# Kernel optimization log

Hardware: AMD Instinct MI355X
Metric: run time of the kernel (lower is better)

Reference implementation:

```python
import jax, jax.numpy as jnp
import numpy as np

VOCAB, EMB, HID = 50000, 256, 512
H = HID // 2            # per-direction hidden size
K = 24                  # tagset size
START, STOP = 22, 23
B, T = 32, 512
NEG = -10000.0


def setup_inputs():
    key = jax.random.key(0)
    ks = jax.random.split(key, 16)
    s = 0.1  # weight scale to keep gates in a sane range
    sentence = jax.random.randint(ks[0], (B, T), 0, VOCAB)
    embedding = jax.random.normal(ks[1], (VOCAB, EMB), jnp.float32)
    w_ih_f = jax.random.normal(ks[2], (4 * H, EMB), jnp.float32) * s
    w_hh_f = jax.random.normal(ks[3], (4 * H, H), jnp.float32) * s
    b_ih_f = jax.random.normal(ks[4], (4 * H,), jnp.float32) * s
    b_hh_f = jax.random.normal(ks[5], (4 * H,), jnp.float32) * s
    w_ih_b = jax.random.normal(ks[6], (4 * H, EMB), jnp.float32) * s
    w_hh_b = jax.random.normal(ks[7], (4 * H, H), jnp.float32) * s
    b_ih_b = jax.random.normal(ks[8], (4 * H,), jnp.float32) * s
    b_hh_b = jax.random.normal(ks[9], (4 * H,), jnp.float32) * s
    w_out = jax.random.normal(ks[10], (K, HID), jnp.float32) * s
    b_out = jax.random.normal(ks[11], (K,), jnp.float32) * s
    transitions = jax.random.normal(ks[12], (K, K), jnp.float32)
    transitions = transitions.at[START, :].set(NEG).at[:, STOP].set(NEG)
    h0 = jax.random.normal(ks[13], (2, B, H), jnp.float32)  # [fwd,bwd] initial h
    c0 = jax.random.normal(ks[14], (2, B, H), jnp.float32)  # [fwd,bwd] initial c
    return {"sentence": sentence, "embedding": embedding,
            "w_ih_f": w_ih_f, "w_hh_f": w_hh_f, "b_ih_f": b_ih_f, "b_hh_f": b_hh_f,
            "w_ih_b": w_ih_b, "w_hh_b": w_hh_b, "b_ih_b": b_ih_b, "b_hh_b": b_hh_b,
            "w_out": w_out, "b_out": b_out, "transitions": transitions,
            "h0": h0, "c0": c0}


def _lstm_dir(x_tbe, w_ih, w_hh, b_ih, b_hh, h0, c0, reverse):
    # x_tbe: [T, B, E]; PyTorch gate order i, f, g, o
    def step(carry, x_t):
        h, c = carry
        gates = x_t @ w_ih.T + b_ih + h @ w_hh.T + b_hh  # [B, 4H]
        i, f, g, o = jnp.split(gates, 4, axis=-1)
        c = jax.nn.sigmoid(f) * c + jax.nn.sigmoid(i) * jnp.tanh(g)
        h = jax.nn.sigmoid(o) * jnp.tanh(c)
        return (h, c), h
    _, hs = jax.lax.scan(step, (h0, c0), x_tbe, reverse=reverse)
    return hs  # [T, B, H]


def _viterbi(feats_tbk, transitions):
    # feats_tbk: [T, B, K]; transitions[next, prev]
    init = jnp.full((B, K), NEG, feats_tbk.dtype).at[:, START].set(0.0)

    def step(fv, feat_t):
        scores = fv[:, None, :] + transitions[None, :, :]  # [B, next, prev]
        bp = jnp.argmax(scores, axis=-1)                   # [B, K]
        fv_new = jnp.max(scores, axis=-1) + feat_t
        return fv_new, bp

    fv, bps = jax.lax.scan(step, init, feats_tbk)  # bps: [T, B, K]
    terminal = fv + transitions[STOP][None, :]
    last_tag = jnp.argmax(terminal, axis=-1)       # [B]
    path_score = jnp.max(terminal, axis=-1)        # [B]

    def back(tag, bp_t):
        prev = jnp.take_along_axis(bp_t, tag[:, None], axis=1)[:, 0]
        return prev, tag
    # process t = T-1 .. 0; carry holds tag at time t, emits it, steps to t-1
    _, path = jax.lax.scan(back, last_tag, bps, reverse=True)  # [T, B]
    return path_score, path.T.astype(jnp.int32)  # [B], [B, T]


def reference(sentence, embedding, w_ih_f, w_hh_f, b_ih_f, b_hh_f,
              w_ih_b, w_hh_b, b_ih_b, b_hh_b, w_out, b_out,
              transitions, h0, c0):
    emb = embedding[sentence]                       # [B, T, EMB]
    x = jnp.transpose(emb, (1, 0, 2))               # [T, B, EMB]
    hf = _lstm_dir(x, w_ih_f, w_hh_f, b_ih_f, b_hh_f, h0[0], c0[0], False)
    hb = _lstm_dir(x, w_ih_b, w_hh_b, b_ih_b, b_hh_b, h0[1], c0[1], True)
    hs = jnp.concatenate([hf, hb], axis=-1)         # [T, B, HID]
    feats = hs @ w_out.T + b_out                    # [T, B, K]
    score, path = _viterbi(feats, transitions)
    return score, path
```

## Files before the change

### kernel.cpp

```cpp
#include <hip/hip_runtime.h>

#define T_LEN 512
#define BATCH 32
#define HDIR  256
#define KTAG  24
#define START_TAG 22
#define STOP_TAG  23
#define NEGV  (-10000.0f)
#define SENTU 0x7FC0DEADu

typedef float vf4 __attribute__((ext_vector_type(4)));

#define XPROJ_OFF   0ull
#define XPROJ_ELEMS (2ull*512*1024*32)
#define FEATS_OFF   (XPROJ_OFF + XPROJ_ELEMS)
#define FEATS_ELEMS (512ull*32*24)
#define HIST_OFF    (FEATS_OFF + FEATS_ELEMS)
#define HIST_ELEMS  (2ull*513*8192)

#define BARRIER_LGKM() asm volatile("s_waitcnt lgkmcnt(0)\n\ts_barrier" ::: "memory")

__device__ __forceinline__ float fsig(float x) {
  return __builtin_amdgcn_rcpf(1.0f + __expf(-x));
}
__device__ __forceinline__ float ftanh(float x) {
  return 2.0f * __builtin_amdgcn_rcpf(1.0f + __expf(-2.0f * x)) - 1.0f;
}
__device__ __forceinline__ unsigned um(unsigned a, unsigned b) { return a < b ? a : b; }

__global__ void k_fill(float* __restrict__ p, int n4) {
  int i = blockIdx.x * blockDim.x + threadIdx.x;
  if (i < n4) {
    float* dst = p + (size_t)i * 4;
    const float sv = __uint_as_float(SENTU);
    vf4 v; v.x = sv; v.y = sv; v.z = sv; v.w = sv;
    asm volatile("global_store_dwordx4 %0, %1, off sc0 sc1"
                 :: "v"(dst), "v"(v) : "memory");
  }
}

__global__ __launch_bounds__(256, 1) void k_main(
    const int* __restrict__ sent, const float* __restrict__ emb,
    const float* __restrict__ wihf, const float* __restrict__ wihb,
    const float* __restrict__ bihf, const float* __restrict__ bhhf,
    const float* __restrict__ bihb, const float* __restrict__ bhhb,
    const float* __restrict__ whhf, const float* __restrict__ whhb,
    const float* __restrict__ h0, const float* __restrict__ c0,
    float* __restrict__ xproj, float* __restrict__ hist)
{
  extern __shared__ float dynpad[];
  __shared__ float As[16][132];
  __shared__ float Bs[16][132];
  __shared__ int   sid[128];
  __shared__ float hl[32 * 256];
  const int bid = blockIdx.x;
  const int tid = threadIdx.x;
  if (sent == (const int*)0) dynpad[0] = 0.f;

  if (bid >= 64) {
    const int idx = bid - 64;
    const int mt_rank = idx >> 4;
    const int sub = idx & 15;
    const int y = sub >> 1;
    const int dir = sub & 1;
    const int mt = (mt_rank & 1) ? (127 - (mt_rank >> 1)) : (mt_rank >> 1);
    const int m0 = mt * 128;
    const int n0 = y * 128;
    const float* __restrict__ W = dir ? wihb : wihf;
    if (tid < 128) {
      int m = m0 + tid;
      sid[tid] = sent[(m & 31) * 512 + (m >> 5)];
    }
    __syncthreads();
    float acc[8][8];
#pragma unroll
    for (int i = 0; i < 8; ++i)
#pragma unroll
      for (int j = 0; j < 8; ++j) acc[i][j] = 0.f;
    const int r = tid >> 1, qq = tid & 1;
    const int ty = tid >> 4, tx = tid & 15;
    for (int k0 = 0; k0 < 256; k0 += 16) {
      const float* ap = &emb[(size_t)sid[r] * 256 + k0 + qq * 8];
      const float* bp = &W[(size_t)(n0 + r) * 256 + k0 + qq * 8];
      float4 a0 = *(const float4*)ap;
      float4 a1 = *(const float4*)(ap + 4);
      float4 b0 = *(const float4*)bp;
      float4 b1 = *(const float4*)(bp + 4);
      __syncthreads();
      As[qq*8+0][r] = a0.x; As[qq*8+1][r] = a0.y; As[qq*8+2][r] = a0.z; As[qq*8+3][r] = a0.w;
      As[qq*8+4][r] = a1.x; As[qq*8+5][r] = a1.y; As[qq*8+6][r] = a1.z; As[qq*8+7][r] = a1.w;
      Bs[qq*8+0][r] = b0.x; Bs[qq*8+1][r] = b0.y; Bs[qq*8+2][r] = b0.z; Bs[qq*8+3][r] = b0.w;
      Bs[qq*8+4][r] = b1.x; Bs[qq*8+5][r] = b1.y; Bs[qq*8+6][r] = b1.z; Bs[qq*8+7][r] = b1.w;
      __syncthreads();
#pragma unroll
      for (int kk = 0; kk < 16; ++kk) {
        float4 av0 = *(const float4*)&As[kk][ty*8];
        float4 av1 = *(const float4*)&As[kk][ty*8+4];
        float4 bv0 = *(const float4*)&Bs[kk][tx*8];
        float4 bv1 = *(const float4*)&Bs[kk][tx*8+4];
        float am[8] = {av0.x,av0.y,av0.z,av0.w,av1.x,av1.y,av1.z,av1.w};
        float bn[8] = {bv0.x,bv0.y,bv0.z,bv0.w,bv1.x,bv1.y,bv1.z,bv1.w};
#pragma unroll
        for (int i = 0; i < 8; ++i)
#pragma unroll
          for (int j = 0; j < 8; ++j)
            acc[i][j] = fmaf(am[i], bn[j], acc[i][j]);
      }
    }
    const float* bi_p = dir ? bihb : bihf;
    const float* bh_p = dir ? bhhb : bhhf;
    float bias[8];
#pragma unroll
    for (int j = 0; j < 8; ++j) { int n = n0 + tx*8 + j; bias[j] = bi_p[n] + bh_p[n]; }
    const int mb = m0 + ty * 8;
    const int tt = mb >> 5, bb = mb & 31;
#pragma unroll
    for (int j = 0; j < 8; ++j) {
      int n = n0 + tx*8 + j;
      float* dst = &xproj[((((size_t)dir*512 + tt)*1024) + n)*32 + bb];
      vf4 o0, o1;
      o0[0] = acc[0][j]+bias[j]; o0[1] = acc[1][j]+bias[j];
      o0[2] = acc[2][j]+bias[j]; o0[3] = acc[3][j]+bias[j];
      o1[0] = acc[4][j]+bias[j]; o1[1] = acc[5][j]+bias[j];
      o1[2] = acc[6][j]+bias[j]; o1[3] = acc[7][j]+bias[j];
      asm volatile(
        "global_store_dwordx4 %0, %2, off sc0 sc1\n\t"
        "global_store_dwordx4 %1, %3, off sc0 sc1"
        :: "v"(dst), "v"(dst + 4), "v"(o0), "v"(o1) : "memory");
    }
    return;
  }

  const int dir = bid >> 5;
  const int slice = bid & 31;
  const int rowg = tid >> 5;
  const int bgrp = (tid >> 3) & 3;
  const int kgrp = tid & 7;
  const int jg = slice * 8 + rowg;
  const float* __restrict__ W = dir ? whhb : whhf;

  float2 w2[4][16];
#pragma unroll
  for (int g = 0; g < 4; ++g)
#pragma unroll
    for (int kk2 = 0; kk2 < 16; ++kk2)
      w2[g][kk2] = *(const float2*)&W[(size_t)(g*256 + jg)*256 + kgrp*32 + 2*kk2];

  float cc[8];
#pragma unroll
  for (int bi = 0; bi < 8; ++bi)
    cc[bi] = c0[(size_t)(dir*32 + bgrp*8 + bi)*256 + jg];

  const int kk = tid & 31;
  const int base_col = tid & ~31;
  const int kw4 = 4*((tid >> 5) & 7);
  const int rot = (4*kgrp + 2*bgrp) & 31;
  float* const histd = hist + (size_t)dir * 513 * 8192;
  float hnew[8];

  for (int s = 0; s < 512; ++s) {
    const int t = dir ? (511 - s) : s;

    vf4 hv[8];
    if (s == 0) {
#pragma unroll
      for (int q = 0; q < 8; ++q)
#pragma unroll
        for (int bl = 0; bl < 4; ++bl)
          hv[q][bl] = h0[(size_t)(dir*32 + 4*q + bl)*256 + tid];
    } else {
      const float* sp = histd + (size_t)s*8192 + (size_t)tid*4;
      const float* p0 = sp;
      const float* p1 = sp + 1024;
      const float* p2 = sp + 2048;
      const float* p3 = sp + 3072;
      const float* p4 = sp + 4096;
      const float* p5 = sp + 5120;
      const float* p6 = sp + 6144;
      const float* p7 = sp + 7168;
      while (true) {
        asm volatile(
          "global_load_dwordx4 %0, %1, off sc0 sc1\n\t"
          "s_waitcnt vmcnt(0)"
          : "=&v"(hv[7]) : "v"(p7) : "memory");
        unsigned z = 0xFFFFFFFFu;
#pragma unroll
        for (int bl = 0; bl < 4; ++bl)
          z = um(z, __float_as_uint(hv[7][bl]) ^ SENTU);
        if (z) break;
        __builtin_amdgcn_s_sleep(1);
      }
      while (true) {
        asm volatile(
          "global_load_dwordx4 %0, %7, off sc0 sc1\n\t"
          "global_load_dwordx4 %1, %8, off sc0 sc1\n\t"
          "global_load_dwordx4 %2, %9, off sc0 sc1\n\t"
          "global_load_dwordx4 %3, %10, off sc0 sc1\n\t"
          "global_load_dwordx4 %4, %11, off sc0 sc1\n\t"
          "global_load_dwordx4 %5, %12, off sc0 sc1\n\t"
          "global_load_dwordx4 %6, %13, off sc0 sc1\n\t"
          "s_waitcnt vmcnt(0)"
          : "=&v"(hv[0]), "=&v"(hv[1]), "=&v"(hv[2]), "=&v"(hv[3]),
            "=&v"(hv[4]), "=&v"(hv[5]), "=&v"(hv[6])
          : "v"(p0), "v"(p1), "v"(p2), "v"(p3),
            "v"(p4), "v"(p5), "v"(p6)
          : "memory");
        unsigned z = 0xFFFFFFFFu;
#pragma unroll
        for (int q = 0; q < 7; ++q)
#pragma unroll
          for (int bl = 0; bl < 4; ++bl)
            z = um(z, __float_as_uint(hv[q][bl]) ^ SENTU);
        if (z) break;
        __builtin_amdgcn_s_sleep(1);
      }
    }

    vf4 xv0, xv1, xv2, xv3, xv4, xv5, xv6, xv7;
    const float* xb = &xproj[((((size_t)dir*512 + t)*1024) + jg)*32 + bgrp*8];
    const float* xa0 = xb;             const float* xa1 = xb + 4;
    const float* xa2 = xb + 8192;      const float* xa3 = xb + 8196;
    const float* xa4 = xb + 16384;     const float* xa5 = xb + 16388;
    const float* xa6 = xb + 24576;     const float* xa7 = xb + 24580;
    if (kgrp == 0) {
      asm volatile(
        "global_load_dwordx4 %0, %8, off sc0 sc1\n\t"
        "global_load_dwordx4 %1, %9, off sc0 sc1\n\t"
        "global_load_dwordx4 %2, %10, off sc0 sc1\n\t"
        "global_load_dwordx4 %3, %11, off sc0 sc1\n\t"
        "global_load_dwordx4 %4, %12, off sc0 sc1\n\t"
        "global_load_dwordx4 %5, %13, off sc0 sc1\n\t"
        "global_load_dwordx4 %6, %14, off sc0 sc1\n\t"
        "global_load_dwordx4 %7, %15, off sc0 sc1"
        : "=&v"(xv0), "=&v"(xv1), "=&v"(xv2), "=&v"(xv3),
          "=&v"(xv4), "=&v"(xv5), "=&v"(xv6), "=&v"(xv7)
        : "v"(xa0), "v"(xa1), "v"(xa2), "v"(xa3),
          "v"(xa4), "v"(xa5), "v"(xa6), "v"(xa7)
        : "memory");
    }

#pragma unroll
    for (int q = 0; q < 8; ++q) {
      const int rwq = (kw4 + 2*((q >> 1) & 3)) & 31;
      const int col = base_col + ((kk + rwq) & 31);
#pragma unroll
      for (int bl = 0; bl < 4; ++bl)
        hl[(4*q + bl)*256 + col] = hv[q][bl];
    }
    BARRIER_LGKM();

    float acc[4][8];
#pragma unroll
    for (int g = 0; g < 4; ++g)
#pragma unroll
      for (int bi = 0; bi < 8; ++bi) acc[g][bi] = 0.f;

    const int hbase = kgrp * 32;
#pragma unroll
    for (int kk2 = 0; kk2 < 16; ++kk2) {
      const int idx = hbase + ((2*kk2 + rot) & 31);
      float2 h2[8];
#pragma unroll
      for (int bi = 0; bi < 8; ++bi)
        h2[bi] = *(const float2*)&hl[(bgrp*8 + bi)*256 + idx];
#pragma unroll
      for (int g = 0; g < 4; ++g)
#pragma unroll
        for (int bi = 0; bi < 8; ++bi) {
          acc[g][bi] = fmaf(w2[g][kk2].x, h2[bi].x, acc[g][bi]);
          acc[g][bi] = fmaf(w2[g][kk2].y, h2[bi].y, acc[g][bi]);
        }
    }

    if (kgrp == 0) {
      asm volatile("s_waitcnt vmcnt(0)"
                   : "+v"(xv0), "+v"(xv1), "+v"(xv2), "+v"(xv3),
                     "+v"(xv4), "+v"(xv5), "+v"(xv6), "+v"(xv7)
                   :: "memory");
      while (true) {
        unsigned z = 0xFFFFFFFFu;
#pragma unroll
        for (int bl = 0; bl < 4; ++bl) {
          z = um(z, __float_as_uint(xv0[bl]) ^ SENTU);
          z = um(z, __float_as_uint(xv1[bl]) ^ SENTU);
          z = um(z, __float_as_uint(xv2[bl]) ^ SENTU);
          z = um(z, __float_as_uint(xv3[bl]) ^ SENTU);
          z = um(z, __float_as_uint(xv4[bl]) ^ SENTU);
          z = um(z, __float_as_uint(xv5[bl]) ^ SENTU);
          z = um(z, __float_as_uint(xv6[bl]) ^ SENTU);
          z = um(z, __float_as_uint(xv7[bl]) ^ SENTU);
        }
        if (z) break;
        __builtin_amdgcn_s_sleep(1);
        asm volatile(
          "global_load_dwordx4 %0, %8, off sc0 sc1\n\t"
          "global_load_dwordx4 %1, %9, off sc0 sc1\n\t"
          "global_load_dwordx4 %2, %10, off sc0 sc1\n\t"
          "global_load_dwordx4 %3, %11, off sc0 sc1\n\t"
          "global_load_dwordx4 %4, %12, off sc0 sc1\n\t"
          "global_load_dwordx4 %5, %13, off sc0 sc1\n\t"
          "global_load_dwordx4 %6, %14, off sc0 sc1\n\t"
          "global_load_dwordx4 %7, %15, off sc0 sc1\n\t"
          "s_waitcnt vmcnt(0)"
          : "=&v"(xv0), "=&v"(xv1), "=&v"(xv2), "=&v"(xv3),
            "=&v"(xv4), "=&v"(xv5), "=&v"(xv6), "=&v"(xv7)
          : "v"(xa0), "v"(xa1), "v"(xa2), "v"(xa3),
            "v"(xa4), "v"(xa5), "v"(xa6), "v"(xa7)
          : "memory");
      }
      acc[0][0]+=xv0[0]; acc[0][1]+=xv0[1]; acc[0][2]+=xv0[2]; acc[0][3]+=xv0[3];
      acc[0][4]+=xv1[0]; acc[0][5]+=xv1[1]; acc[0][6]+=xv1[2]; acc[0][7]+=xv1[3];
      acc[1][0]+=xv2[0]; acc[1][1]+=xv2[1]; acc[1][2]+=xv2[2]; acc[1][3]+=xv2[3];
      acc[1][4]+=xv3[0]; acc[1][5]+=xv3[1]; acc[1][6]+=xv3[2]; acc[1][7]+=xv3[3];
      acc[2][0]+=xv4[0]; acc[2][1]+=xv4[1]; acc[2][2]+=xv4[2]; acc[2][3]+=xv4[3];
      acc[2][4]+=xv5[0]; acc[2][5]+=xv5[1]; acc[2][6]+=xv5[2]; acc[2][7]+=xv5[3];
      acc[3][0]+=xv6[0]; acc[3][1]+=xv6[1]; acc[3][2]+=xv6[2]; acc[3][3]+=xv6[3];
      acc[3][4]+=xv7[0]; acc[3][5]+=xv7[1]; acc[3][6]+=xv7[2]; acc[3][7]+=xv7[3];
    }
#pragma unroll
    for (int g = 0; g < 4; ++g)
#pragma unroll
      for (int bi = 0; bi < 8; ++bi) {
        float v = acc[g][bi];
        v += __shfl_xor(v, 1, 64);
        v += __shfl_xor(v, 2, 64);
        v += __shfl_xor(v, 4, 64);
        acc[g][bi] = v;
      }

#pragma unroll
    for (int bi = 0; bi < 8; ++bi) {
      float ig = fsig(acc[0][bi]);
      float fg = fsig(acc[1][bi]);
      float gg = ftanh(acc[2][bi]);
      float og = fsig(acc[3][bi]);
      cc[bi] = fg * cc[bi] + ig * gg;
      hnew[bi] = og * ftanh(cc[bi]);
    }

    if (kgrp == 0) {
      float* dp  = histd + (size_t)(s + 1)*8192 + ((size_t)(2*bgrp)*256 + jg)*4;
      float* dp2 = dp + 1024;
      vf4 s0; s0.x = hnew[0]; s0.y = hnew[1]; s0.z = hnew[2]; s0.w = hnew[3];
      vf4 s1; s1.x = hnew[4]; s1.y = hnew[5]; s1.z = hnew[6]; s1.w = hnew[7];
      asm volatile(
        "global_store_dwordx4 %0, %2, off sc0 sc1\n\t"
        "global_store_dwordx4 %1, %3, off sc0 sc1"
        :: "v"(dp), "v"(dp2), "v"(s0), "v"(s1) : "memory");
    }

    BARRIER_LGKM();
  }
}

__global__ __launch_bounds__(256) void k_feats(
    const float* __restrict__ hist, const float* __restrict__ wout,
    const float* __restrict__ bout, float* __restrict__ feats)
{
  const int t = blockIdx.x;
  const int tid = threadIdx.x;
  __shared__ float hlds[32 * 516];
#pragma unroll
  for (int dir = 0; dir < 2; ++dir) {
    const int slot = dir ? (512 - t) : (t + 1);
    const float* sp = hist + ((size_t)dir*513 + slot)*8192;
#pragma unroll
    for (int q = 0; q < 8; ++q) {
      vf4 v = *(const vf4*)&sp[(size_t)(q*256 + tid)*4];
      float* d = &hlds[(4*q)*516 + dir*256 + tid];
      d[0*516] = v.x; d[1*516] = v.y; d[2*516] = v.z; d[3*516] = v.w;
    }
  }
  __syncthreads();
  const int b = tid >> 3, ks = tid & 7;
#pragma unroll
  for (int kt = 0; kt < 3; ++kt) {
    int k = kt * 8 + ks;
    float acc = bout[k];
    const float* wr = wout + (size_t)k * 512;
#pragma unroll 8
    for (int kk = 0; kk < 512; kk += 4) {
      float4 h4 = *(const float4*)&hlds[b * 516 + kk];
      float4 w4 = *(const float4*)&wr[kk];
      acc += h4.x*w4.x + h4.y*w4.y + h4.z*w4.z + h4.w*w4.w;
    }
    feats[((size_t)t * 32 + b) * 24 + k] = acc;
  }
}

__global__ __launch_bounds__(64) void k_viterbi(
    const float* __restrict__ feats, const float* __restrict__ trans,
    float* __restrict__ out)
{
  const int b = blockIdx.x;
  const int lane = threadIdx.x;
  const int k = lane;
  __shared__ float fvl[2][32];
  __shared__ float pathb[512];
  __shared__ unsigned char bcol[512 * 24];
  float trr[24];
  if (k < 24) {
#pragma unroll
    for (int pv = 0; pv < 24; ++pv) trr[pv] = trans[k * 24 + pv];
  }
  if (k < 32) fvl[0][k] = (k == START_TAG) ? 0.f : NEGV;
  if (k < 32) fvl[1][k] = NEGV;
  __syncthreads();
  float fcur = (k < 24) ? feats[b * 24 + k] : 0.f;
  int q = 0;
  for (int t = 0; t < 512; ++t) {
    float fnext = (t < 511 && k < 24) ? feats[(size_t)(t + 1) * 768 + b * 24 + k] : 0.f;
    float fvp[24];
    {
      const float4* fp4 = (const float4*)&fvl[q][0];
#pragma unroll
      for (int i = 0; i < 6; ++i) {
        float4 v = fp4[i];
        fvp[i*4+0] = v.x; fvp[i*4+1] = v.y; fvp[i*4+2] = v.z; fvp[i*4+3] = v.w;
      }
    }
    float best = -3.4e38f; int bp = 0;
#pragma unroll
    for (int pv = 0; pv < 24; ++pv) {
      float v = fvp[pv] + trr[pv];
      if (v > best) { best = v; bp = pv; }
    }
    if (k < 24) {
      fvl[q ^ 1][k] = best + fcur;
      bcol[t * 24 + k] = (unsigned char)bp;
    }
    fcur = fnext;
    q ^= 1;
    __syncthreads();
  }
  if (lane == 0) {
    float best = -3.4e38f; int bt = 0;
#pragma unroll
    for (int kk = 0; kk < 24; ++kk) {
      float v = fvl[q][kk] + trans[STOP_TAG * 24 + kk];
      if (v > best) { best = v; bt = kk; }
    }
    out[b] = best;
    pathb[511] = (float)bt;
    int tag = bt;
    for (int t = 511; t >= 1; --t) {
      tag = bcol[t * 24 + tag];
      pathb[t - 1] = (float)tag;
    }
  }
  __syncthreads();
#pragma unroll
  for (int it = 0; it < 8; ++it)
    out[32 + (size_t)b * 512 + it * 64 + lane] = pathb[it * 64 + lane];
}

extern "C" void kernel_launch(void* const* d_in, const int* in_sizes, int n_in,
                              void* d_out, int out_size, void* d_ws, size_t ws_size,
                              hipStream_t stream) {
  (void)in_sizes; (void)n_in; (void)out_size; (void)ws_size;
  const int*   sent = (const int*)d_in[0];
  const float* emb  = (const float*)d_in[1];
  const float* wihf = (const float*)d_in[2];
  const float* whhf = (const float*)d_in[3];
  const float* bihf = (const float*)d_in[4];
  const float* bhhf = (const float*)d_in[5];
  const float* wihb = (const float*)d_in[6];
  const float* whhb = (const float*)d_in[7];
  const float* bihb = (const float*)d_in[8];
  const float* bhhb = (const float*)d_in[9];
  const float* wout = (const float*)d_in[10];
  const float* bout = (const float*)d_in[11];
  const float* trans= (const float*)d_in[12];
  const float* h0   = (const float*)d_in[13];
  const float* c0   = (const float*)d_in[14];

  float* ws     = (float*)d_ws;
  float* xproj  = ws + XPROJ_OFF;
  float* feats  = ws + FEATS_OFF;
  float* hist   = ws + HIST_OFF;

  const int n4 = (int)((XPROJ_ELEMS + FEATS_ELEMS + HIST_ELEMS) / 4);
  k_fill<<<(n4 + 255) / 256, 256, 0, stream>>>(ws, n4);
  k_main<<<2112, 256, 32768, stream>>>(sent, emb, wihf, wihb,
                                       bihf, bhhf, bihb, bhhb,
                                       whhf, whhb, h0, c0, xproj, hist);
  k_feats<<<512, 256, 0, stream>>>(hist, wout, bout, feats);
  k_viterbi<<<32, 64, 0, stream>>>(feats, trans, (float*)d_out);
}
```

Baseline: 4.387 ms.

## Fuse output projection into persistent kernel and replace sentinel-fill of xproj with per-tile flags

Moves the hidden-to-tag projection into extra blocks of the main persistent kernel. These blocks spin on the history buffer and compute feats as each timestep's forward and backward states become available, overlapping with the recurrence. The recurrent blocks no longer poll every xproj element for a sentinel. Instead, each GEMM tile writes a completion flag into the unused hist slot-0 region, and readers poll that flag every four timesteps. This lets the fill kernel touch only hist instead of the large xproj buffer. The change also register-prefetches the next K-slice in the input-projection GEMM, at the cost of more spin-polling blocks and extra resident work competing with the latency-critical recurrence.

```diff
diff --git a/kernel.cpp b/kernel.cpp
--- a/kernel.cpp
+++ b/kernel.cpp
@@ -46,18 +46,20 @@
     const float* __restrict__ bihb, const float* __restrict__ bhhb,
     const float* __restrict__ whhf, const float* __restrict__ whhb,
     const float* __restrict__ h0, const float* __restrict__ c0,
-    float* __restrict__ xproj, float* __restrict__ hist)
+    const float* __restrict__ wout, const float* __restrict__ bout,
+    float* __restrict__ xproj, float* __restrict__ feats,
+    float* __restrict__ hist)
 {
   extern __shared__ float dynpad[];
-  __shared__ float As[16][132];
-  __shared__ float Bs[16][132];
-  __shared__ int   sid[128];
-  __shared__ float hl[32 * 256];
+  __shared__ float smem[12544];
   const int bid = blockIdx.x;
   const int tid = threadIdx.x;
   if (sent == (const int*)0) dynpad[0] = 0.f;
 
-  if (bid >= 64) {
+  if (bid >= 64 && bid < 2112) {
+    float (*As)[132] = (float (*)[132])(smem);
+    float (*Bs)[132] = (float (*)[132])(smem + 2112);
+    int* sid = (int*)(smem + 4224);
     const int idx = bid - 64;
     const int mt_rank = idx >> 4;
     const int sub = idx & 15;
@@ -79,19 +81,27 @@
       for (int j = 0; j < 8; ++j) acc[i][j] = 0.f;
     const int r = tid >> 1, qq = tid & 1;
     const int ty = tid >> 4, tx = tid & 15;
+    const float* ap = &emb[(size_t)sid[r] * 256 + qq * 8];
+    const float* bp = &W[(size_t)(n0 + r) * 256 + qq * 8];
+    float4 a0 = *(const float4*)(ap);
+    float4 a1 = *(const float4*)(ap + 4);
+    float4 b0 = *(const float4*)(bp);
+    float4 b1 = *(const float4*)(bp + 4);
     for (int k0 = 0; k0 < 256; k0 += 16) {
-      const float* ap = &emb[(size_t)sid[r] * 256 + k0 + qq * 8];
-      const float* bp = &W[(size_t)(n0 + r) * 256 + k0 + qq * 8];
-      float4 a0 = *(const float4*)ap;
-      float4 a1 = *(const float4*)(ap + 4);
-      float4 b0 = *(const float4*)bp;
-      float4 b1 = *(const float4*)(bp + 4);
       __syncthreads();
       As[qq*8+0][r] = a0.x; As[qq*8+1][r] = a0.y; As[qq*8+2][r] = a0.z; As[qq*8+3][r] = a0.w;
       As[qq*8+4][r] = a1.x; As[qq*8+5][r] = a1.y; As[qq*8+6][r] = a1.z; As[qq*8+7][r] = a1.w;
       Bs[qq*8+0][r] = b0.x; Bs[qq*8+1][r] = b0.y; Bs[qq*8+2][r] = b0.z; Bs[qq*8+3][r] = b0.w;
       Bs[qq*8+4][r] = b1.x; Bs[qq*8+5][r] = b1.y; Bs[qq*8+6][r] = b1.z; Bs[qq*8+7][r] = b1.w;
       __syncthreads();
+      if (k0 + 16 < 256) {
+        const float* ap2 = ap + k0 + 16;
+        const float* bp2 = bp + k0 + 16;
+        a0 = *(const float4*)(ap2);
+        a1 = *(const float4*)(ap2 + 4);
+        b0 = *(const float4*)(bp2);
+        b1 = *(const float4*)(bp2 + 4);
+      }
 #pragma unroll
       for (int kk = 0; kk < 16; ++kk) {
         float4 av0 = *(const float4*)&As[kk][ty*8];
@@ -128,9 +138,94 @@
         "global_store_dwordx4 %1, %3, off sc0 sc1"
         :: "v"(dst), "v"(dst + 4), "v"(o0), "v"(o1) : "memory");
     }
+    asm volatile("s_waitcnt vmcnt(0)" ::: "memory");
+    __syncthreads();
+    if (tid == 0) {
+      float* fp = hist + (size_t)dir * 1024 + (size_t)mt * 8 + y;
+      const float z = 0.f;
+      asm volatile("global_store_dword %0, %1, off sc0 sc1"
+                   :: "v"(fp), "v"(z) : "memory");
+    }
     return;
   }
 
+  if (bid >= 2112) {
+    const int f = bid - 2112;
+    const int t = (f & 1) ? (256 + (f >> 1)) : (255 - (f >> 1));
+    float* hlds = smem;
+    const float* sF = hist + ((size_t)0*513 + (t + 1)) * 8192;
+    const float* sB = hist + ((size_t)1*513 + (512 - t)) * 8192;
+    {
+      const int p = tid & 31;
+      const float* pp = (((tid >> 5) & 1) ? sB : sF) + 32 * p;
+      while (true) {
+        float v;
+        asm volatile("global_load_dword %0, %1, off sc0 sc1\n\ts_waitcnt vmcnt(0)"
+                     : "=&v"(v) : "v"(pp) : "memory");
+        int bad = (__float_as_uint(v) == SENTU) ? 1 : 0;
+        if (!__any(bad)) break;
+        __builtin_amdgcn_s_sleep(64);
+      }
+    }
+    const int b = tid >> 3, ks = tid & 7;
+    float accv[3];
+    for (int dir2 = 0; dir2 < 2; ++dir2) {
+      const float* sp = (dir2 ? sB : sF) + (size_t)tid * 4;
+      vf4 v[8];
+      while (true) {
+        asm volatile(
+          "global_load_dwordx4 %0, %8, off sc0 sc1\n\t"
+          "global_load_dwordx4 %1, %9, off sc0 sc1\n\t"
+          "global_load_dwordx4 %2, %10, off sc0 sc1\n\t"
+          "global_load_dwordx4 %3, %11, off sc0 sc1\n\t"
+          "global_load_dwordx4 %4, %12, off sc0 sc1\n\t"
+          "global_load_dwordx4 %5, %13, off sc0 sc1\n\t"
+          "global_load_dwordx4 %6, %14, off sc0 sc1\n\t"
+          "global_load_dwordx4 %7, %15, off sc0 sc1\n\t"
+          "s_waitcnt vmcnt(0)"
+          : "=&v"(v[0]), "=&v"(v[1]), "=&v"(v[2]), "=&v"(v[3]),
+            "=&v"(v[4]), "=&v"(v[5]), "=&v"(v[6]), "=&v"(v[7])
+          : "v"(sp), "v"(sp+1024), "v"(sp+2048), "v"(sp+3072),
+            "v"(sp+4096), "v"(sp+5120), "v"(sp+6144), "v"(sp+7168)
+          : "memory");
+        unsigned z = 0xFFFFFFFFu;
+#pragma unroll
+        for (int q = 0; q < 8; ++q)
+#pragma unroll
+          for (int bl = 0; bl < 4; ++bl)
+            z = um(z, __float_as_uint(v[q][bl]) ^ SENTU);
+        if (z) break;
+        __builtin_amdgcn_s_sleep(16);
+      }
+#pragma unroll
+      for (int q = 0; q < 8; ++q)
+#pragma unroll
+        for (int bl = 0; bl < 4; ++bl)
+          hlds[(4*q + bl)*258 + tid] = v[q][bl];
+      __syncthreads();
+#pragma unroll
+      for (int kt = 0; kt < 3; ++kt) {
+        const int k = kt * 8 + ks;
+        if (dir2 == 0) accv[kt] = bout[k];
+        const float* wr = wout + (size_t)k * 512 + dir2 * 256;
+        float a = accv[kt];
+#pragma unroll 8
+        for (int kk = 0; kk < 256; kk += 4) {
+          float4 h4 = *(const float4*)&hlds[b * 258 + kk];
+          float4 w4 = *(const float4*)&wr[kk];
+          a += h4.x*w4.x + h4.y*w4.y + h4.z*w4.z + h4.w*w4.w;
+        }
+        accv[kt] = a;
+      }
+      __syncthreads();
+    }
+#pragma unroll
+    for (int kt = 0; kt < 3; ++kt)
+      feats[((size_t)t * 32 + b) * 24 + kt * 8 + ks] = accv[kt];
+    return;
+  }
+
+  float* hl = smem + 4352;
   const int dir = bid >> 5;
   const int slice = bid & 31;
   const int rowg = tid >> 5;
@@ -216,27 +311,35 @@
       }
     }
 
-    vf4 xv0, xv1, xv2, xv3, xv4, xv5, xv6, xv7;
-    const float* xb = &xproj[((((size_t)dir*512 + t)*1024) + jg)*32 + bgrp*8];
-    const float* xa0 = xb;             const float* xa1 = xb + 4;
-    const float* xa2 = xb + 8192;      const float* xa3 = xb + 8196;
-    const float* xa4 = xb + 16384;     const float* xa5 = xb + 16388;
-    const float* xa6 = xb + 24576;     const float* xa7 = xb + 24580;
+    float xpr[4][8];
     if (kgrp == 0) {
-      asm volatile(
-        "global_load_dwordx4 %0, %8, off sc0 sc1\n\t"
-        "global_load_dwordx4 %1, %9, off sc0 sc1\n\t"
-        "global_load_dwordx4 %2, %10, off sc0 sc1\n\t"
-        "global_load_dwordx4 %3, %11, off sc0 sc1\n\t"
-        "global_load_dwordx4 %4, %12, off sc0 sc1\n\t"
-        "global_load_dwordx4 %5, %13, off sc0 sc1\n\t"
-        "global_load_dwordx4 %6, %14, off sc0 sc1\n\t"
-        "global_load_dwordx4 %7, %15, off sc0 sc1"
-        : "=&v"(xv0), "=&v"(xv1), "=&v"(xv2), "=&v"(xv3),
-          "=&v"(xv4), "=&v"(xv5), "=&v"(xv6), "=&v"(xv7)
-        : "v"(xa0), "v"(xa1), "v"(xa2), "v"(xa3),
-          "v"(xa4), "v"(xa5), "v"(xa6), "v"(xa7)
-        : "memory");
+      if ((t & 3) == (dir ? 3 : 0)) {
+        const float* fp = hist + (size_t)dir*1024 + (size_t)(t >> 2)*8;
+        while (true) {
+          vf4 f0, f1;
+          asm volatile(
+            "global_load_dwordx4 %0, %2, off sc0 sc1\n\t"
+            "global_load_dwordx4 %1, %3, off sc0 sc1\n\t"
+            "s_waitcnt vmcnt(0)"
+            : "=&v"(f0), "=&v"(f1) : "v"(fp), "v"(fp + 4) : "memory");
+          unsigned bad = 0u;
+#pragma unroll
+          for (int l = 0; l < 4; ++l) {
+            bad |= (__float_as_uint(f0[l]) == SENTU) ? 1u : 0u;
+            bad |= (__float_as_uint(f1[l]) == SENTU) ? 1u : 0u;
+          }
+          if (!bad) break;
+          __builtin_amdgcn_s_sleep(2);
+        }
+      }
+#pragma unroll
+      for (int g = 0; g < 4; ++g) {
+        const float* xp = &xproj[((((size_t)dir*512 + t)*1024) + g*256 + jg)*32 + bgrp*8];
+        float4 x0 = *(const float4*)xp;
+        float4 x1 = *(const float4*)(xp + 4);
+        xpr[g][0]=x0.x; xpr[g][1]=x0.y; xpr[g][2]=x0.z; xpr[g][3]=x0.w;
+        xpr[g][4]=x1.x; xpr[g][5]=x1.y; xpr[g][6]=x1.z; xpr[g][7]=x1.w;
+      }
     }
 
 #pragma unroll
@@ -273,49 +376,10 @@
     }
 
     if (kgrp == 0) {
-      asm volatile("s_waitcnt vmcnt(0)"
-                   : "+v"(xv0), "+v"(xv1), "+v"(xv2), "+v"(xv3),
-                     "+v"(xv4), "+v"(xv5), "+v"(xv6), "+v"(xv7)
-                   :: "memory");
-      while (true) {
-        unsigned z = 0xFFFFFFFFu;
-#pragma unroll
-        for (int bl = 0; bl < 4; ++bl) {
-          z = um(z, __float_as_uint(xv0[bl]) ^ SENTU);
-          z = um(z, __float_as_uint(xv1[bl]) ^ SENTU);
-          z = um(z, __float_as_uint(xv2[bl]) ^ SENTU);
-          z = um(z, __float_as_uint(xv3[bl]) ^ SENTU);
-          z = um(z, __float_as_uint(xv4[bl]) ^ SENTU);
-          z = um(z, __float_as_uint(xv5[bl]) ^ SENTU);
-          z = um(z, __float_as_uint(xv6[bl]) ^ SENTU);
-          z = um(z, __float_as_uint(xv7[bl]) ^ SENTU);
-        }
-        if (z) break;
-        __builtin_amdgcn_s_sleep(1);
-        asm volatile(
-          "global_load_dwordx4 %0, %8, off sc0 sc1\n\t"
-          "global_load_dwordx4 %1, %9, off sc0 sc1\n\t"
-          "global_load_dwordx4 %2, %10, off sc0 sc1\n\t"
-          "global_load_dwordx4 %3, %11, off sc0 sc1\n\t"
-          "global_load_dwordx4 %4, %12, off sc0 sc1\n\t"
-          "global_load_dwordx4 %5, %13, off sc0 sc1\n\t"
-          "global_load_dwordx4 %6, %14, off sc0 sc1\n\t"
-          "global_load_dwordx4 %7, %15, off sc0 sc1\n\t"
-          "s_waitcnt vmcnt(0)"
-          : "=&v"(xv0), "=&v"(xv1), "=&v"(xv2), "=&v"(xv3),
-            "=&v"(xv4), "=&v"(xv5), "=&v"(xv6), "=&v"(xv7)
-          : "v"(xa0), "v"(xa1), "v"(xa2), "v"(xa3),
-            "v"(xa4), "v"(xa5), "v"(xa6), "v"(xa7)
-          : "memory");
-      }
-      acc[0][0]+=xv0[0]; acc[0][1]+=xv0[1]; acc[0][2]+=xv0[2]; acc[0][3]+=xv0[3];
-      acc[0][4]+=xv1[0]; acc[0][5]+=xv1[1]; acc[0][6]+=xv1[2]; acc[0][7]+=xv1[3];
-      acc[1][0]+=xv2[0]; acc[1][1]+=xv2[1]; acc[1][2]+=xv2[2]; acc[1][3]+=xv2[3];
-      acc[1][4]+=xv3[0]; acc[1][5]+=xv3[1]; acc[1][6]+=xv3[2]; acc[1][7]+=xv3[3];
-      acc[2][0]+=xv4[0]; acc[2][1]+=xv4[1]; acc[2][2]+=xv4[2]; acc[2][3]+=xv4[3];
-      acc[2][4]+=xv5[0]; acc[2][5]+=xv5[1]; acc[2][6]+=xv5[2]; acc[2][7]+=xv5[3];
-      acc[3][0]+=xv6[0]; acc[3][1]+=xv6[1]; acc[3][2]+=xv6[2]; acc[3][3]+=xv6[3];
-      acc[3][4]+=xv7[0]; acc[3][5]+=xv7[1]; acc[3][6]+=xv7[2]; acc[3][7]+=xv7[3];
+#pragma unroll
+      for (int g = 0; g < 4; ++g)
+#pragma unroll
+        for (int bi = 0; bi < 8; ++bi) acc[g][bi] += xpr[g][bi];
     }
 #pragma unroll
     for (int g = 0; g < 4; ++g)
@@ -350,41 +414,6 @@
     }
 
     BARRIER_LGKM();
-  }
-}
-
-__global__ __launch_bounds__(256) void k_feats(
-    const float* __restrict__ hist, const float* __restrict__ wout,
-    const float* __restrict__ bout, float* __restrict__ feats)
-{
-  const int t = blockIdx.x;
-  const int tid = threadIdx.x;
-  __shared__ float hlds[32 * 516];
-#pragma unroll
-  for (int dir = 0; dir < 2; ++dir) {
-    const int slot = dir ? (512 - t) : (t + 1);
-    const float* sp = hist + ((size_t)dir*513 + slot)*8192;
-#pragma unroll
-    for (int q = 0; q < 8; ++q) {
-      vf4 v = *(const vf4*)&sp[(size_t)(q*256 + tid)*4];
-      float* d = &hlds[(4*q)*516 + dir*256 + tid];
-      d[0*516] = v.x; d[1*516] = v.y; d[2*516] = v.z; d[3*516] = v.w;
-    }
-  }
-  __syncthreads();
-  const int b = tid >> 3, ks = tid & 7;
-#pragma unroll
-  for (int kt = 0; kt < 3; ++kt) {
-    int k = kt * 8 + ks;
-    float acc = bout[k];
-    const float* wr = wout + (size_t)k * 512;
-#pragma unroll 8
-    for (int kk = 0; kk < 512; kk += 4) {
-      float4 h4 = *(const float4*)&hlds[b * 516 + kk];
-      float4 w4 = *(const float4*)&wr[kk];
-      acc += h4.x*w4.x + h4.y*w4.y + h4.z*w4.z + h4.w*w4.w;
-    }
-    feats[((size_t)t * 32 + b) * 24 + k] = acc;
   }
 }
 
@@ -479,11 +508,11 @@
   float* feats  = ws + FEATS_OFF;
   float* hist   = ws + HIST_OFF;
 
-  const int n4 = (int)((XPROJ_ELEMS + FEATS_ELEMS + HIST_ELEMS) / 4);
-  k_fill<<<(n4 + 255) / 256, 256, 0, stream>>>(ws, n4);
-  k_main<<<2112, 256, 32768, stream>>>(sent, emb, wihf, wihb,
+  const int n4 = (int)(HIST_ELEMS / 4);
+  k_fill<<<(n4 + 255) / 256, 256, 0, stream>>>(hist, n4);
+  k_main<<<2624, 256, 32768, stream>>>(sent, emb, wihf, wihb,
                                        bihf, bhhf, bihb, bhhb,
-                                       whhf, whhb, h0, c0, xproj, hist);
-  k_feats<<<512, 256, 0, stream>>>(hist, wout, bout, feats);
+                                       whhf, whhb, h0, c0,
+                                       wout, bout, xproj, feats, hist);
   k_viterbi<<<32, 64, 0, stream>>>(feats, trans, (float*)d_out);
 }
```

Result: faster. 4.196 ms (-4.4%).
